# Performance work log

Measured on AMD Instinct MI355X. Metric: run time of the kernel, lower is better.

Reference implementation:

```python
import jax, jax.numpy as jnp
import numpy as np

B, S, D, H = 4, 2048, 1024, 16
DK = D // H

def setup_inputs() -> dict:
    key = jax.random.key(0)
    ks = jax.random.split(key, 11)
    sc = 1.0 / np.sqrt(D)
    return {
        "query": jax.random.normal(ks[0], (B, S, D), jnp.float32),
        "key_": jax.random.normal(ks[1], (B, S, D), jnp.float32),
        "value": jax.random.normal(ks[2], (B, S, D), jnp.float32),
        "Wq": jax.random.normal(ks[3], (D, D), jnp.float32) * sc,
        "bq": jnp.zeros((D,), jnp.float32),
        "Wk": jax.random.normal(ks[4], (D, D), jnp.float32) * sc,
        "bk": jnp.zeros((D,), jnp.float32),
        "Wv": jax.random.normal(ks[5], (D, D), jnp.float32) * sc,
        "bv": jnp.zeros((D,), jnp.float32),
        "Wo": jax.random.normal(ks[6], (D, D), jnp.float32) * sc,
        "bo": jnp.zeros((D,), jnp.float32),
    }

def reference(query, key_, value, Wq, bq, Wk, bk, Wv, bv, Wo, bo):
    def proj(x, W, b):
        # [B,S,D] -> [B,H,S,DK]
        y = x @ W.T + b
        return y.reshape(B, S, H, DK).transpose(0, 2, 1, 3)
    q = proj(query, Wq, bq)
    k = proj(key_, Wk, bk)
    v = proj(value, Wv, bv)
    scores = jnp.einsum("bhqd,bhkd->bhqk", q, k) / jnp.sqrt(jnp.float32(DK))
    p = jax.nn.softmax(scores, axis=-1)
    x = jnp.einsum("bhqk,bhkd->bhqd", p, v)
    x = x.transpose(0, 2, 1, 3).reshape(B, S, D)
    return x @ Wo.T + bo
```

## Files before the change

kernel.cpp:

```cpp
#include <hip/hip_runtime.h>
#include <math.h>

#define Bc 4
#define Sc 2048
#define Dc 1024
#define Hc 16
#define DKc 64

typedef __bf16 bf16;
typedef __bf16 bf16x4 __attribute__((ext_vector_type(4)));
typedef __bf16 bf16x8 __attribute__((ext_vector_type(8)));
typedef float  floatx4 __attribute__((ext_vector_type(4)));

__device__ __forceinline__ void load_lds16(const void* g, void* l) {
    __builtin_amdgcn_global_load_lds((const __attribute__((address_space(1))) void*)g,
                                     (__attribute__((address_space(3))) void*)l, 16, 0, 0);
}

#define MFMA16(a, b, c) __builtin_amdgcn_mfma_f32_16x16x32_bf16(a, b, c, 0, 0, 0)

template<int MODE>
__device__ __forceinline__ void gemm_body(const bf16* __restrict__ A,
                                          const bf16* __restrict__ W,
                                          const float* __restrict__ bias,
                                          void* __restrict__ out,
                                          bf16* As, bf16* Bs) {
    constexpr int N = Dc, K = Dc;
    const int t  = threadIdx.x;
    const int w  = t >> 6;
    const int l  = t & 63;
    const int m0 = blockIdx.y * 128;
    const int n0 = blockIdx.x * 128;
    const int wm = (w >> 1) * 64;
    const int wn = (w & 1) * 64;
    const int srow = l >> 2;
    const int scol = (l & 3) * 8;
    const int fl = l & 15;
    const int fq = l >> 4;

    floatx4 acc[4][4];
#pragma unroll
    for (int i = 0; i < 4; i++)
#pragma unroll
        for (int j = 0; j < 4; j++)
            acc[i][j] = (floatx4){0.f, 0.f, 0.f, 0.f};

    for (int k0 = 0; k0 < K; k0 += 32) {
#pragma unroll
        for (int i = 0; i < 2; i++) {
            const int inst = w + i * 4;
            load_lds16(A + (size_t)(m0 + inst * 16 + srow) * K + k0 + scol, As + inst * 512);
            load_lds16(W + (size_t)(n0 + inst * 16 + srow) * K + k0 + scol, Bs + inst * 512);
        }
        __syncthreads();

        bf16x8 af[4], bfr[4];
#pragma unroll
        for (int tm = 0; tm < 4; tm++)
            af[tm] = *(const bf16x8*)(As + (wm + tm * 16 + fl) * 32 + fq * 8);
#pragma unroll
        for (int tn = 0; tn < 4; tn++)
            bfr[tn] = *(const bf16x8*)(Bs + (wn + tn * 16 + fl) * 32 + fq * 8);
#pragma unroll
        for (int tm = 0; tm < 4; tm++)
#pragma unroll
            for (int tn = 0; tn < 4; tn++)
                acc[tm][tn] = MFMA16(af[tm], bfr[tn], acc[tm][tn]);
        __syncthreads();
    }

#pragma unroll
    for (int tn = 0; tn < 4; tn++) {
        const int n = n0 + wn + tn * 16 + fl;
        const float bv = bias[n];
#pragma unroll
        for (int tm = 0; tm < 4; tm++) {
            const int mb = m0 + wm + tm * 16 + fq * 4;
            if (MODE == 0) {
                float* O = (float*)out;
#pragma unroll
                for (int r = 0; r < 4; r++)
                    O[(size_t)(mb + r) * N + n] = acc[tm][tn][r] + bv;
            } else if (MODE == 1) {
                bf16* O = (bf16*)out;
#pragma unroll
                for (int r = 0; r < 4; r++)
                    O[(size_t)(mb + r) * N + n] = (bf16)(acc[tm][tn][r] + bv);
            } else {
                const int h = n >> 6, dk = n & 63;
                const int b = mb >> 11, s = mb & 2047;
                bf16* O = (bf16*)out + ((size_t)((b * Hc + h) * DKc + dk)) * Sc + s;
                bf16x4 pk = {(bf16)(acc[tm][tn][0] + bv), (bf16)(acc[tm][tn][1] + bv),
                             (bf16)(acc[tm][tn][2] + bv), (bf16)(acc[tm][tn][3] + bv)};
                *(bf16x4*)O = pk;
            }
        }
    }
}

__global__ __launch_bounds__(256) void gemm_qkv(
    const bf16* __restrict__ Aq, const bf16* __restrict__ Ak, const bf16* __restrict__ Av,
    const bf16* __restrict__ Wqb, const bf16* __restrict__ Wkb, const bf16* __restrict__ Wvb,
    const float* __restrict__ bqs, const float* __restrict__ bk, const float* __restrict__ bv,
    bf16* __restrict__ Oq, bf16* __restrict__ Ok, bf16* __restrict__ Ov) {
    __shared__ bf16 As[128 * 32];
    __shared__ bf16 Bs[128 * 32];
    const int sel = blockIdx.z;
    if (sel == 0)      gemm_body<1>(Aq, Wqb, bqs, Oq, As, Bs);
    else if (sel == 1) gemm_body<1>(Ak, Wkb, bk,  Ok, As, Bs);
    else               gemm_body<2>(Av, Wvb, bv,  Ov, As, Bs);
}

__global__ __launch_bounds__(256) void gemm_out_k(const bf16* __restrict__ A,
                                                  const bf16* __restrict__ W,
                                                  const float* __restrict__ bias,
                                                  float* __restrict__ out) {
    __shared__ bf16 As[128 * 32];
    __shared__ bf16 Bs[128 * 32];
    gemm_body<0>(A, W, bias, out, As, Bs);
}

#define PSTRIDE 36

#define STAGE(d, kt) do {                                                     \
    load_lds16(Kb + (size_t)((kt) + w * 8 + krow) * Dc + kchunk * 8,          \
               &Kbuf[d][w * 512]);                                            \
    load_lds16(Vb + (size_t)(w * 16 + vrow) * Sc + (kt) + vchunk * 8,         \
               &Vbuf[d][w * 512]);                                            \
} while (0)

#define QK(d) do {                                                            \
    bf16x8 kf00 = *(const bf16x8*)&Kbuf[d][fl * 64        + ((fq ^ kx) * 8)];       \
    bf16x8 kf01 = *(const bf16x8*)&Kbuf[d][fl * 64        + (((4 + fq) ^ kx) * 8)]; \
    bf16x8 kf10 = *(const bf16x8*)&Kbuf[d][(16 + fl) * 64 + ((fq ^ kx) * 8)];       \
    bf16x8 kf11 = *(const bf16x8*)&Kbuf[d][(16 + fl) * 64 + (((4 + fq) ^ kx) * 8)]; \
    floatx4 z;                                                                \
    z = (floatx4){-8.f, -8.f, -8.f, -8.f};                                    \
    z = MFMA16(kf00, q00, z); s00 = MFMA16(kf01, q01, z);                     \
    z = (floatx4){-8.f, -8.f, -8.f, -8.f};                                    \
    z = MFMA16(kf00, q10, z); s01 = MFMA16(kf01, q11, z);                     \
    z = (floatx4){-8.f, -8.f, -8.f, -8.f};                                    \
    z = MFMA16(kf10, q00, z); s10 = MFMA16(kf11, q01, z);                     \
    z = (floatx4){-8.f, -8.f, -8.f, -8.f};                                    \
    z = MFMA16(kf10, q10, z); s11 = MFMA16(kf11, q11, z);                     \
} while (0)

#define EXP1(S, L, OFF) do {                                                  \
    float p0 = __expf(S[0]), p1 = __expf(S[1]);                               \
    float p2 = __expf(S[2]), p3 = __expf(S[3]);                               \
    L += (p0 + p1) + (p2 + p3);                                               \
    bf16x4 pk = {(bf16)p0, (bf16)p1, (bf16)p2, (bf16)p3};                     \
    *(bf16x4*)(pwb + (OFF)) = pk;                                             \
} while (0)

#define EXPW() do {                                                           \
    EXP1(s00, l0, 0 * 16 * PSTRIDE + 0);                                      \
    EXP1(s10, l0, 0 * 16 * PSTRIDE + 16);                                     \
    EXP1(s01, l1, 1 * 16 * PSTRIDE + 0);                                      \
    EXP1(s11, l1, 1 * 16 * PSTRIDE + 16);                                     \
} while (0)

#define PV(d) do {                                                            \
    bf16x8 vf0 = *(const bf16x8*)&Vbuf[d][fl * 32        + ((fq ^ svf) * 8)]; \
    bf16x8 vf1 = *(const bf16x8*)&Vbuf[d][(16 + fl) * 32 + ((fq ^ svf) * 8)]; \
    bf16x8 vf2 = *(const bf16x8*)&Vbuf[d][(32 + fl) * 32 + ((fq ^ svf) * 8)]; \
    bf16x8 vf3 = *(const bf16x8*)&Vbuf[d][(48 + fl) * 32 + ((fq ^ svf) * 8)]; \
    bf16x8 pf0 = *(const bf16x8*)(prb);                                       \
    bf16x8 pf1 = *(const bf16x8*)(prb + 16 * PSTRIDE);                        \
    o00 = MFMA16(vf0, pf0, o00); o01 = MFMA16(vf0, pf1, o01);                 \
    o10 = MFMA16(vf1, pf0, o10); o11 = MFMA16(vf1, pf1, o11);                 \
    o20 = MFMA16(vf2, pf0, o20); o21 = MFMA16(vf2, pf1, o21);                 \
    o30 = MFMA16(vf3, pf0, o30); o31 = MFMA16(vf3, pf1, o31);                 \
} while (0)

__global__ __launch_bounds__(256, 3) void attn_mfma(const bf16* __restrict__ Q,
                                                    const bf16* __restrict__ Kg,
                                                    const bf16* __restrict__ Vt,
                                                    bf16* __restrict__ X) {
    __shared__ bf16 Kbuf[2][32 * 64];
    __shared__ bf16 Vbuf[2][64 * 32];
    __shared__ bf16 P2[4][32 * PSTRIDE];

    const int bh = blockIdx.x & 63;
    const int qb = blockIdx.x >> 6;
    const int b = bh >> 4, h = bh & 15;

    const int w  = threadIdx.x >> 6;
    const int l  = threadIdx.x & 63;
    const int fl = l & 15;
    const int fq = l >> 4;
    const int q0i = qb * 128 + w * 32;

    const int krow   = l >> 3;
    const int kchunk = (l & 7) ^ krow;
    const int vrow   = l >> 2;
    const int vchunk = (l & 3) ^ ((vrow + (vrow >> 2)) & 3);
    const int kx  = fl & 7;
    const int svf = (fl + (fl >> 2)) & 3;

    const bf16* Qb = Q  + (size_t)b * Sc * Dc + h * DKc;
    const bf16* Kb = Kg + (size_t)b * Sc * Dc + h * DKc;
    const bf16* Vb = Vt + (size_t)((b * Hc + h) * DKc) * Sc;

    bf16* pwb       = &P2[w][fl * PSTRIDE + fq * 4];
    const bf16* prb = &P2[w][fl * PSTRIDE + fq * 8];

    bf16x8 q00 = *(const bf16x8*)(Qb + (size_t)(q0i + fl) * Dc + fq * 8);
    bf16x8 q01 = *(const bf16x8*)(Qb + (size_t)(q0i + fl) * Dc + 32 + fq * 8);
    bf16x8 q10 = *(const bf16x8*)(Qb + (size_t)(q0i + 16 + fl) * Dc + fq * 8);
    bf16x8 q11 = *(const bf16x8*)(Qb + (size_t)(q0i + 16 + fl) * Dc + 32 + fq * 8);

    floatx4 o00 = {0.f, 0.f, 0.f, 0.f}, o01 = o00, o10 = o00, o11 = o00;
    floatx4 o20 = o00, o21 = o00, o30 = o00, o31 = o00;
    float l0 = 0.f, l1 = 0.f;
    floatx4 s00, s01, s10, s11;

    STAGE(0, 0);
    __syncthreads();

    for (int kt = 0; kt < Sc; kt += 64) {
        STAGE(1, kt + 32);
        QK(0); EXPW(); PV(0);
        __syncthreads();
        if (kt + 64 < Sc) STAGE(0, kt + 64);
        QK(1); EXPW(); PV(1);
        __syncthreads();
    }

    {
        float lsum = l0;
        lsum += __shfl_xor(lsum, 16);
        lsum += __shfl_xor(lsum, 32);
        const float inv = 1.f / lsum;
        bf16* xp = X + ((size_t)(b * Sc + q0i + fl)) * Dc + h * DKc + fq * 4;
        floatx4 o;
        bf16x4 pk;
        o = o00 * inv; pk = (bf16x4){(bf16)o[0], (bf16)o[1], (bf16)o[2], (bf16)o[3]}; *(bf16x4*)(xp)      = pk;
        o = o10 * inv; pk = (bf16x4){(bf16)o[0], (bf16)o[1], (bf16)o[2], (bf16)o[3]}; *(bf16x4*)(xp + 16) = pk;
        o = o20 * inv; pk = (bf16x4){(bf16)o[0], (bf16)o[1], (bf16)o[2], (bf16)o[3]}; *(bf16x4*)(xp + 32) = pk;
        o = o30 * inv; pk = (bf16x4){(bf16)o[0], (bf16)o[1], (bf16)o[2], (bf16)o[3]}; *(bf16x4*)(xp + 48) = pk;
    }
    {
        float lsum = l1;
        lsum += __shfl_xor(lsum, 16);
        lsum += __shfl_xor(lsum, 32);
        const float inv = 1.f / lsum;
        bf16* xp = X + ((size_t)(b * Sc + q0i + 16 + fl)) * Dc + h * DKc + fq * 4;
        floatx4 o;
        bf16x4 pk;
        o = o01 * inv; pk = (bf16x4){(bf16)o[0], (bf16)o[1], (bf16)o[2], (bf16)o[3]}; *(bf16x4*)(xp)      = pk;
        o = o11 * inv; pk = (bf16x4){(bf16)o[0], (bf16)o[1], (bf16)o[2], (bf16)o[3]}; *(bf16x4*)(xp + 16) = pk;
        o = o21 * inv; pk = (bf16x4){(bf16)o[0], (bf16)o[1], (bf16)o[2], (bf16)o[3]}; *(bf16x4*)(xp + 32) = pk;
        o = o31 * inv; pk = (bf16x4){(bf16)o[0], (bf16)o[1], (bf16)o[2], (bf16)o[3]}; *(bf16x4*)(xp + 48) = pk;
    }
}

__global__ __launch_bounds__(256) void cast_qkv(const float* __restrict__ q,
                                                const float* __restrict__ k,
                                                const float* __restrict__ v,
                                                bf16* __restrict__ oq,
                                                bf16* __restrict__ ok,
                                                bf16* __restrict__ ov, int n4) {
    const int sel = blockIdx.z;
    const float* src = sel == 0 ? q : sel == 1 ? k : v;
    bf16* dst = sel == 0 ? oq : sel == 1 ? ok : ov;
    int i = blockIdx.x * 256 + threadIdx.x;
    if (i < n4) {
        const float4 vv = ((const float4*)src)[i];
        bf16x4 o = {(bf16)vv.x, (bf16)vv.y, (bf16)vv.z, (bf16)vv.w};
        ((bf16x4*)dst)[i] = o;
    }
}

__global__ __launch_bounds__(256) void cast_w(const float* __restrict__ wq,
                                              const float* __restrict__ wk,
                                              const float* __restrict__ wv,
                                              const float* __restrict__ wo,
                                              bf16* __restrict__ o0, bf16* __restrict__ o1,
                                              bf16* __restrict__ o2, bf16* __restrict__ o3,
                                              int n4) {
    const int sel = blockIdx.z;
    const float* src = sel == 0 ? wq : sel == 1 ? wk : sel == 2 ? wv : wo;
    bf16* dst = sel == 0 ? o0 : sel == 1 ? o1 : sel == 2 ? o2 : o3;
    const float scale = sel == 0 ? 0.125f : 1.f;
    int i = blockIdx.x * 256 + threadIdx.x;
    if (i < n4) {
        const float4 vv = ((const float4*)src)[i];
        bf16x4 o = {(bf16)(vv.x * scale), (bf16)(vv.y * scale),
                    (bf16)(vv.z * scale), (bf16)(vv.w * scale)};
        ((bf16x4*)dst)[i] = o;
    }
}

__global__ __launch_bounds__(256) void scale_vec(const float* __restrict__ s,
                                                 float* __restrict__ d, int n, float sc) {
    int i = blockIdx.x * 256 + threadIdx.x;
    if (i < n) d[i] = s[i] * sc;
}

extern "C" void kernel_launch(void* const* d_in, const int* in_sizes, int n_in,
                              void* d_out, int out_size, void* d_ws, size_t ws_size,
                              hipStream_t stream) {
    const float* query = (const float*)d_in[0];
    const float* key_  = (const float*)d_in[1];
    const float* value = (const float*)d_in[2];
    const float* Wq    = (const float*)d_in[3];
    const float* bq    = (const float*)d_in[4];
    const float* Wk    = (const float*)d_in[5];
    const float* bk    = (const float*)d_in[6];
    const float* Wv    = (const float*)d_in[7];
    const float* bv    = (const float*)d_in[8];
    const float* Wo    = (const float*)d_in[9];
    const float* bo    = (const float*)d_in[10];

    const size_t nSD = (size_t)Bc * Sc * Dc;
    const size_t nWW = (size_t)Dc * Dc;

    char* ws = (char*)d_ws;
    bf16* qbf = (bf16*)ws;              ws += nSD * 2;
    bf16* kbf = (bf16*)ws;              ws += nSD * 2;
    bf16* vbf = (bf16*)ws;              ws += nSD * 2;
    bf16* wqb = (bf16*)ws;              ws += nWW * 2;
    bf16* wkb = (bf16*)ws;              ws += nWW * 2;
    bf16* wvb = (bf16*)ws;              ws += nWW * 2;
    bf16* wob = (bf16*)ws;              ws += nWW * 2;
    bf16* Qw  = (bf16*)ws;              ws += nSD * 2;
    bf16* Kw  = (bf16*)ws;              ws += nSD * 2;
    bf16* Vtw = (bf16*)ws;              ws += nSD * 2;
    bf16* Xw  = (bf16*)ws;              ws += nSD * 2;
    float* bqs = (float*)ws;            ws += Dc * 4;

    dim3 gc3((int)(nSD / 4 / 256), 1, 3);
    cast_qkv<<<gc3, 256, 0, stream>>>(query, key_, value, qbf, kbf, vbf, (int)(nSD / 4));
    dim3 gc4((int)(nWW / 4 / 256), 1, 4);
    cast_w<<<gc4, 256, 0, stream>>>(Wq, Wk, Wv, Wo, wqb, wkb, wvb, wob, (int)(nWW / 4));
    scale_vec<<<4, 256, 0, stream>>>(bq, bqs, Dc, 0.125f);

    dim3 ggrid(Dc / 128, Bc * Sc / 128, 3);
    gemm_qkv<<<ggrid, 256, 0, stream>>>(qbf, kbf, vbf, wqb, wkb, wvb,
                                        bqs, bk, bv, Qw, Kw, Vtw);

    attn_mfma<<<(Sc / 128) * Hc * Bc, 256, 0, stream>>>(Qw, Kw, Vtw, Xw);

    dim3 gout(Dc / 128, Bc * Sc / 128);
    gemm_out_k<<<gout, 256, 0, stream>>>(Xw, wob, bo, (float*)d_out);
}
```

Measured before the change: 388.9 us.

## Rewrite attention inner loop with 32x32 MFMA and register-resident P via permlane swaps

The attention kernel moves from 16x16x32 to 32x32x16 bf16 MFMA tiles and keeps the softmax probabilities in registers. It uses permlane32_swap to reshape them into the B-operand layout instead of round-tripping through an LDS P buffer. Key/value staging tiles double to 64 keys per buffer, s_setprio brackets the MFMA groups, and the launch bound rises to 4 blocks per CU. The aim is fewer LDS writes and reads and less per-MFMA overhead, at the cost of a larger accumulator register footprint and more LDS per block, which could hurt occupancy.

```diff
diff --git a/kernel.cpp b/kernel.cpp
--- a/kernel.cpp
+++ b/kernel.cpp
@@ -8,9 +8,11 @@
 #define DKc 64
 
 typedef __bf16 bf16;
+typedef __bf16 bf16x2 __attribute__((ext_vector_type(2)));
 typedef __bf16 bf16x4 __attribute__((ext_vector_type(4)));
 typedef __bf16 bf16x8 __attribute__((ext_vector_type(8)));
 typedef float  floatx4 __attribute__((ext_vector_type(4)));
+typedef float  floatx16 __attribute__((ext_vector_type(16)));
 
 __device__ __forceinline__ void load_lds16(const void* g, void* l) {
     __builtin_amdgcn_global_load_lds((const __attribute__((address_space(1))) void*)g,
@@ -18,6 +20,7 @@
 }
 
 #define MFMA16(a, b, c) __builtin_amdgcn_mfma_f32_16x16x32_bf16(a, b, c, 0, 0, 0)
+#define MFMA32(a, b, c) __builtin_amdgcn_mfma_f32_32x32x16_bf16(a, b, c, 0, 0, 0)
 
 template<int MODE>
 __device__ __forceinline__ void gemm_body(const bf16* __restrict__ A,
@@ -120,138 +123,149 @@
     gemm_body<0>(A, W, bias, out, As, Bs);
 }
 
-#define PSTRIDE 36
-
-#define STAGE(d, kt) do {                                                     \
-    load_lds16(Kb + (size_t)((kt) + w * 8 + krow) * Dc + kchunk * 8,          \
-               &Kbuf[d][w * 512]);                                            \
-    load_lds16(Vb + (size_t)(w * 16 + vrow) * Sc + (kt) + vchunk * 8,         \
-               &Vbuf[d][w * 512]);                                            \
+
+__device__ __forceinline__ unsigned pkpair(float a, float b) {
+    union { bf16x2 v; unsigned u; } x;
+    x.v = (bf16x2){(bf16)a, (bf16)b};
+    return x.u;
+}
+
+__device__ __forceinline__ bf16x8 frag4(unsigned a, unsigned b, unsigned c, unsigned d) {
+    union { unsigned u[4]; bf16x8 v; } x;
+    x.u[0] = a; x.u[1] = b; x.u[2] = c; x.u[3] = d;
+    return x.v;
+}
+
+__device__ __forceinline__ floatx16 splat16(float v) {
+    floatx16 r;
+#pragma unroll
+    for (int i = 0; i < 16; ++i) r[i] = v;
+    return r;
+}
+
+#define PSWAP(x, y) do {                                                      \
+    auto _r = __builtin_amdgcn_permlane32_swap((int)(x), (int)(y), false, false); \
+    (x) = (unsigned)_r[0]; (y) = (unsigned)_r[1];                             \
 } while (0)
 
-#define QK(d) do {                                                            \
-    bf16x8 kf00 = *(const bf16x8*)&Kbuf[d][fl * 64        + ((fq ^ kx) * 8)];       \
-    bf16x8 kf01 = *(const bf16x8*)&Kbuf[d][fl * 64        + (((4 + fq) ^ kx) * 8)]; \
-    bf16x8 kf10 = *(const bf16x8*)&Kbuf[d][(16 + fl) * 64 + ((fq ^ kx) * 8)];       \
-    bf16x8 kf11 = *(const bf16x8*)&Kbuf[d][(16 + fl) * 64 + (((4 + fq) ^ kx) * 8)]; \
-    floatx4 z;                                                                \
-    z = (floatx4){-8.f, -8.f, -8.f, -8.f};                                    \
-    z = MFMA16(kf00, q00, z); s00 = MFMA16(kf01, q01, z);                     \
-    z = (floatx4){-8.f, -8.f, -8.f, -8.f};                                    \
-    z = MFMA16(kf00, q10, z); s01 = MFMA16(kf01, q11, z);                     \
-    z = (floatx4){-8.f, -8.f, -8.f, -8.f};                                    \
-    z = MFMA16(kf10, q00, z); s10 = MFMA16(kf11, q01, z);                     \
-    z = (floatx4){-8.f, -8.f, -8.f, -8.f};                                    \
-    z = MFMA16(kf10, q10, z); s11 = MFMA16(kf11, q11, z);                     \
+#define STAGE(dst, kt) do {                                                   \
+    load_lds16(Kb + (size_t)((kt) + w * 16 + r8) * Dc + c8 * 8,               \
+               &Kbuf[dst][w * 1024]);                                         \
+    load_lds16(Kb + (size_t)((kt) + w * 16 + 8 + r8) * Dc + c8 * 8,           \
+               &Kbuf[dst][w * 1024 + 512]);                                   \
+    load_lds16(Vb + (size_t)(w * 16 + r8) * Sc + (kt) + c8 * 8,               \
+               &Vbuf[dst][w * 1024]);                                         \
+    load_lds16(Vb + (size_t)(w * 16 + 8 + r8) * Sc + (kt) + c8 * 8,           \
+               &Vbuf[dst][w * 1024 + 512]);                                   \
 } while (0)
 
-#define EXP1(S, L, OFF) do {                                                  \
-    float p0 = __expf(S[0]), p1 = __expf(S[1]);                               \
-    float p2 = __expf(S[2]), p3 = __expf(S[3]);                               \
-    L += (p0 + p1) + (p2 + p3);                                               \
-    bf16x4 pk = {(bf16)p0, (bf16)p1, (bf16)p2, (bf16)p3};                     \
-    *(bf16x4*)(pwb + (OFF)) = pk;                                             \
+#define SOFT() do {                                                           \
+    float pp[16];                                                             \
+    _Pragma("unroll")                                                         \
+    for (int r = 0; r < 16; ++r) pp[r] = __expf(sacc[r]);                     \
+    lsum += ((pp[0] + pp[1]) + (pp[2] + pp[3]))                               \
+          + ((pp[4] + pp[5]) + (pp[6] + pp[7]))                               \
+          + ((pp[8] + pp[9]) + (pp[10] + pp[11]))                             \
+          + ((pp[12] + pp[13]) + (pp[14] + pp[15]));                          \
+    unsigned d0 = pkpair(pp[0], pp[1]),   d1 = pkpair(pp[2], pp[3]);          \
+    unsigned d2 = pkpair(pp[4], pp[5]),   d3 = pkpair(pp[6], pp[7]);          \
+    PSWAP(d0, d2); PSWAP(d1, d3);                                             \
+    pf0 = frag4(d0, d1, d2, d3);                                              \
+    unsigned e0 = pkpair(pp[8], pp[9]),   e1 = pkpair(pp[10], pp[11]);        \
+    unsigned e2 = pkpair(pp[12], pp[13]), e3 = pkpair(pp[14], pp[15]);        \
+    PSWAP(e0, e2); PSWAP(e1, e3);                                             \
+    pf1 = frag4(e0, e1, e2, e3);                                              \
 } while (0)
 
-#define EXPW() do {                                                           \
-    EXP1(s00, l0, 0 * 16 * PSTRIDE + 0);                                      \
-    EXP1(s10, l0, 0 * 16 * PSTRIDE + 16);                                     \
-    EXP1(s01, l1, 1 * 16 * PSTRIDE + 0);                                      \
-    EXP1(s11, l1, 1 * 16 * PSTRIDE + 16);                                     \
+#define TILE(d, T) do {                                                       \
+    const bf16* Kp = &Kbuf[d][((T) * 32 + ky) * 64];                          \
+    const bf16x8 kf0 = *(const bf16x8*)(Kp + ((b5 ^ sw7) * 8));               \
+    const bf16x8 kf1 = *(const bf16x8*)(Kp + (((2 + b5) ^ sw7) * 8));         \
+    const bf16x8 kf2 = *(const bf16x8*)(Kp + (((4 + b5) ^ sw7) * 8));         \
+    const bf16x8 kf3 = *(const bf16x8*)(Kp + (((6 + b5) ^ sw7) * 8));         \
+    __builtin_amdgcn_s_setprio(1);                                            \
+    sacc = MFMA32(kf0, qf0, z16);                                             \
+    sacc = MFMA32(kf1, qf1, sacc);                                            \
+    sacc = MFMA32(kf2, qf2, sacc);                                            \
+    sacc = MFMA32(kf3, qf3, sacc);                                            \
+    __builtin_amdgcn_s_setprio(0);                                            \
+    SOFT();                                                                   \
+    const bf16* Va = &Vbuf[d][ky * 64];                                       \
+    const bf16* Vc = Va + 32 * 64;                                            \
+    const bf16x8 vf00 = *(const bf16x8*)(Va + (((((T) << 2) + b5) ^ sw7) * 8));      \
+    const bf16x8 vf01 = *(const bf16x8*)(Va + (((((T) << 2) + 2 + b5) ^ sw7) * 8));  \
+    const bf16x8 vf10 = *(const bf16x8*)(Vc + (((((T) << 2) + b5) ^ sw7) * 8));      \
+    const bf16x8 vf11 = *(const bf16x8*)(Vc + (((((T) << 2) + 2 + b5) ^ sw7) * 8));  \
+    __builtin_amdgcn_s_setprio(1);                                            \
+    oa = MFMA32(vf00, pf0, oa);                                               \
+    oa = MFMA32(vf01, pf1, oa);                                               \
+    ob = MFMA32(vf10, pf0, ob);                                               \
+    ob = MFMA32(vf11, pf1, ob);                                               \
+    __builtin_amdgcn_s_setprio(0);                                            \
 } while (0)
 
-#define PV(d) do {                                                            \
-    bf16x8 vf0 = *(const bf16x8*)&Vbuf[d][fl * 32        + ((fq ^ svf) * 8)]; \
-    bf16x8 vf1 = *(const bf16x8*)&Vbuf[d][(16 + fl) * 32 + ((fq ^ svf) * 8)]; \
-    bf16x8 vf2 = *(const bf16x8*)&Vbuf[d][(32 + fl) * 32 + ((fq ^ svf) * 8)]; \
-    bf16x8 vf3 = *(const bf16x8*)&Vbuf[d][(48 + fl) * 32 + ((fq ^ svf) * 8)]; \
-    bf16x8 pf0 = *(const bf16x8*)(prb);                                       \
-    bf16x8 pf1 = *(const bf16x8*)(prb + 16 * PSTRIDE);                        \
-    o00 = MFMA16(vf0, pf0, o00); o01 = MFMA16(vf0, pf1, o01);                 \
-    o10 = MFMA16(vf1, pf0, o10); o11 = MFMA16(vf1, pf1, o11);                 \
-    o20 = MFMA16(vf2, pf0, o20); o21 = MFMA16(vf2, pf1, o21);                 \
-    o30 = MFMA16(vf3, pf0, o30); o31 = MFMA16(vf3, pf1, o31);                 \
-} while (0)
-
-__global__ __launch_bounds__(256, 3) void attn_mfma(const bf16* __restrict__ Q,
+__global__ __launch_bounds__(256, 4) void attn_mfma(const bf16* __restrict__ Q,
                                                     const bf16* __restrict__ Kg,
                                                     const bf16* __restrict__ Vt,
                                                     bf16* __restrict__ X) {
-    __shared__ bf16 Kbuf[2][32 * 64];
-    __shared__ bf16 Vbuf[2][64 * 32];
-    __shared__ bf16 P2[4][32 * PSTRIDE];
+    __shared__ bf16 Kbuf[2][64 * 64];
+    __shared__ bf16 Vbuf[2][64 * 64];
 
     const int bh = blockIdx.x & 63;
     const int qb = blockIdx.x >> 6;
     const int b = bh >> 4, h = bh & 15;
 
-    const int w  = threadIdx.x >> 6;
-    const int l  = threadIdx.x & 63;
-    const int fl = l & 15;
-    const int fq = l >> 4;
+    const int w   = threadIdx.x >> 6;
+    const int l   = threadIdx.x & 63;
+    const int ky  = l & 31;
+    const int b5  = l >> 5;
+    const int sw7 = l & 7;
+    const int r8  = l >> 3;
+    const int c8  = (l & 7) ^ r8;
     const int q0i = qb * 128 + w * 32;
-
-    const int krow   = l >> 3;
-    const int kchunk = (l & 7) ^ krow;
-    const int vrow   = l >> 2;
-    const int vchunk = (l & 3) ^ ((vrow + (vrow >> 2)) & 3);
-    const int kx  = fl & 7;
-    const int svf = (fl + (fl >> 2)) & 3;
 
     const bf16* Qb = Q  + (size_t)b * Sc * Dc + h * DKc;
     const bf16* Kb = Kg + (size_t)b * Sc * Dc + h * DKc;
     const bf16* Vb = Vt + (size_t)((b * Hc + h) * DKc) * Sc;
 
-    bf16* pwb       = &P2[w][fl * PSTRIDE + fq * 4];
-    const bf16* prb = &P2[w][fl * PSTRIDE + fq * 8];
-
-    bf16x8 q00 = *(const bf16x8*)(Qb + (size_t)(q0i + fl) * Dc + fq * 8);
-    bf16x8 q01 = *(const bf16x8*)(Qb + (size_t)(q0i + fl) * Dc + 32 + fq * 8);
-    bf16x8 q10 = *(const bf16x8*)(Qb + (size_t)(q0i + 16 + fl) * Dc + fq * 8);
-    bf16x8 q11 = *(const bf16x8*)(Qb + (size_t)(q0i + 16 + fl) * Dc + 32 + fq * 8);
-
-    floatx4 o00 = {0.f, 0.f, 0.f, 0.f}, o01 = o00, o10 = o00, o11 = o00;
-    floatx4 o20 = o00, o21 = o00, o30 = o00, o31 = o00;
-    float l0 = 0.f, l1 = 0.f;
-    floatx4 s00, s01, s10, s11;
+    const bf16* Qrow = Qb + (size_t)(q0i + ky) * Dc + 8 * b5;
+    const bf16x8 qf0 = *(const bf16x8*)(Qrow);
+    const bf16x8 qf1 = *(const bf16x8*)(Qrow + 16);
+    const bf16x8 qf2 = *(const bf16x8*)(Qrow + 32);
+    const bf16x8 qf3 = *(const bf16x8*)(Qrow + 48);
+
+    const floatx16 z16 = splat16(-8.f);
+    floatx16 oa = splat16(0.f), ob = splat16(0.f);
+    floatx16 sacc;
+    bf16x8 pf0, pf1;
+    float lsum = 0.f;
 
     STAGE(0, 0);
     __syncthreads();
 
-    for (int kt = 0; kt < Sc; kt += 64) {
-        STAGE(1, kt + 32);
-        QK(0); EXPW(); PV(0);
+#pragma unroll 1
+    for (int kt = 0; kt < Sc; kt += 128) {
+        STAGE(1, kt + 64);
+        TILE(0, 0);
+        TILE(0, 1);
         __syncthreads();
-        if (kt + 64 < Sc) STAGE(0, kt + 64);
-        QK(1); EXPW(); PV(1);
+        if (kt + 128 < Sc) STAGE(0, kt + 128);
+        TILE(1, 0);
+        TILE(1, 1);
         __syncthreads();
     }
 
-    {
-        float lsum = l0;
-        lsum += __shfl_xor(lsum, 16);
-        lsum += __shfl_xor(lsum, 32);
-        const float inv = 1.f / lsum;
-        bf16* xp = X + ((size_t)(b * Sc + q0i + fl)) * Dc + h * DKc + fq * 4;
-        floatx4 o;
-        bf16x4 pk;
-        o = o00 * inv; pk = (bf16x4){(bf16)o[0], (bf16)o[1], (bf16)o[2], (bf16)o[3]}; *(bf16x4*)(xp)      = pk;
-        o = o10 * inv; pk = (bf16x4){(bf16)o[0], (bf16)o[1], (bf16)o[2], (bf16)o[3]}; *(bf16x4*)(xp + 16) = pk;
-        o = o20 * inv; pk = (bf16x4){(bf16)o[0], (bf16)o[1], (bf16)o[2], (bf16)o[3]}; *(bf16x4*)(xp + 32) = pk;
-        o = o30 * inv; pk = (bf16x4){(bf16)o[0], (bf16)o[1], (bf16)o[2], (bf16)o[3]}; *(bf16x4*)(xp + 48) = pk;
-    }
-    {
-        float lsum = l1;
-        lsum += __shfl_xor(lsum, 16);
-        lsum += __shfl_xor(lsum, 32);
-        const float inv = 1.f / lsum;
-        bf16* xp = X + ((size_t)(b * Sc + q0i + 16 + fl)) * Dc + h * DKc + fq * 4;
-        floatx4 o;
-        bf16x4 pk;
-        o = o01 * inv; pk = (bf16x4){(bf16)o[0], (bf16)o[1], (bf16)o[2], (bf16)o[3]}; *(bf16x4*)(xp)      = pk;
-        o = o11 * inv; pk = (bf16x4){(bf16)o[0], (bf16)o[1], (bf16)o[2], (bf16)o[3]}; *(bf16x4*)(xp + 16) = pk;
-        o = o21 * inv; pk = (bf16x4){(bf16)o[0], (bf16)o[1], (bf16)o[2], (bf16)o[3]}; *(bf16x4*)(xp + 32) = pk;
-        o = o31 * inv; pk = (bf16x4){(bf16)o[0], (bf16)o[1], (bf16)o[2], (bf16)o[3]}; *(bf16x4*)(xp + 48) = pk;
+    lsum += __shfl_xor(lsum, 32);
+    const float inv = 1.f / lsum;
+    bf16* xp = X + ((size_t)(b * Sc + q0i + ky)) * Dc + h * DKc + b5 * 4;
+#pragma unroll
+    for (int g = 0; g < 4; ++g) {
+        bf16x4 pa = {(bf16)(oa[4 * g + 0] * inv), (bf16)(oa[4 * g + 1] * inv),
+                     (bf16)(oa[4 * g + 2] * inv), (bf16)(oa[4 * g + 3] * inv)};
+        *(bf16x4*)(xp + g * 8) = pa;
+        bf16x4 pb = {(bf16)(ob[4 * g + 0] * inv), (bf16)(ob[4 * g + 1] * inv),
+                     (bf16)(ob[4 * g + 2] * inv), (bf16)(ob[4 * g + 3] * inv)};
+        *(bf16x4*)(xp + 32 + g * 8) = pb;
     }
 }
 
```

New measurement: 688.1 us. 1.77x slower.
